# Kernel tuning notes

Measured on AMD Instinct MI355X. Metric: run time of the kernel, lower is better.

## Reference

```python
import math
import jax, jax.numpy as jnp
import numpy as np

B, T, D_MODEL = 4, 2048, 1024
H, HD = 16, 64            # head_dim = d_model // n_heads
NF = 128                  # n_features
EPS = 1e-6
INV_SQRT_NF = 1.0 / math.sqrt(NF)


def make_orf(key, head_dim, n_features, dtype=jnp.float32):
    """Orthogonal Random Features: QR-orthogonalized gaussian blocks, scaled by sqrt(d)."""
    n_blocks = math.ceil(n_features / head_dim)
    keys = jax.random.split(key, n_blocks)
    blocks = []
    for k in keys:
        g = jax.random.normal(k, (head_dim, head_dim), dtype)
        qm, _ = jnp.linalg.qr(g)
        blocks.append(qm)
    W = jnp.concatenate(blocks, axis=1)[:, :n_features]
    return W * jnp.asarray(math.sqrt(head_dim), dtype)


def setup_inputs() -> dict:
    key = jax.random.key(0)
    k0, k1, k2, k3, k4, k5 = jax.random.split(key, 6)
    s = 1.0 / math.sqrt(D_MODEL)  # torch Linear default init scale
    x = jax.random.normal(k0, (B, T, D_MODEL), jnp.float32)
    Wq = jax.random.uniform(k1, (D_MODEL, H * HD), jnp.float32, -s, s)
    Wk = jax.random.uniform(k2, (D_MODEL, H * HD), jnp.float32, -s, s)
    Wv = jax.random.uniform(k3, (D_MODEL, H * HD), jnp.float32, -s, s)
    Wo = jax.random.uniform(k4, (H * HD, D_MODEL), jnp.float32, -s, s)
    W_feat = make_orf(k5, HD, NF)  # (HD, NF), fresh random buffer (not learned)
    return {"x": x, "Wq": Wq, "Wk": Wk, "Wv": Wv, "Wo": Wo, "W_feat": W_feat}


def _favor_plus(x, W):
    """phi(x) = exp(x.W - ||x||^2/2) / sqrt(NF); x:(B,H,T,HD) -> (B,H,T,NF)."""
    sq = 0.5 * jnp.sum(x * x, axis=-1, keepdims=True)
    return jnp.exp(x @ W - sq) * INV_SQRT_NF


def _causal_linear_attention(qp, kp, v):
    """Causal linear attention scan. qp,kp:(B,H,T,NF), v:(B,H,T,HD) -> (B,H,T,HD)."""
    Bb, Hh = qp.shape[0], qp.shape[1]

    def step(carry, qkv):
        S, z = carry  # S:(B,H,NF,HD), z:(B,H,NF)
        q_t, k_t, v_t = qkv
        S = S + jnp.einsum('bhd,bhe->bhde', k_t, v_t)
        z = z + k_t
        num = jnp.einsum('bhd,bhde->bhe', q_t, S)
        den = jnp.einsum('bhd,bhd->bh', q_t, z) + EPS
        return (S, z), num / den[..., None]

    S0 = jnp.zeros((Bb, Hh, NF, HD), qp.dtype)
    z0 = jnp.zeros((Bb, Hh, NF), qp.dtype)
    xs = (jnp.moveaxis(qp, 2, 0), jnp.moveaxis(kp, 2, 0), jnp.moveaxis(v, 2, 0))
    _, ys = jax.lax.scan(step, (S0, z0), xs)  # ys: (T,B,H,HD)
    return jnp.moveaxis(ys, 0, 2)  # (B,H,T,HD)


def reference(x, Wq, Wk, Wv, Wo, W_feat):
    Bb, Tt, _ = x.shape

    def heads(W):
        return (x @ W).reshape(Bb, Tt, H, HD).transpose(0, 2, 1, 3)  # (B,H,T,HD)

    q, k, v = heads(Wq), heads(Wk), heads(Wv)
    qp = _favor_plus(q, W_feat)
    kp = _favor_plus(k, W_feat)
    y = _causal_linear_attention(qp, kp, v)           # (B,H,T,HD)
    y = y.transpose(0, 2, 1, 3).reshape(Bb, Tt, H * HD)
    return y @ Wo
```

## Files before the change

kernel.cpp:

```cpp
#include <hip/hip_runtime.h>
#include <hip/hip_bf16.h>

typedef unsigned int u32;
typedef unsigned short u16;
typedef __bf16 bf16x8 __attribute__((ext_vector_type(8)));
typedef float f32x4 __attribute__((ext_vector_type(4)));

__device__ __forceinline__ float b2f(u16 s){ union{u32 x; float f;} c; c.x = ((u32)s) << 16; return c.f; }
__device__ __forceinline__ float b2f_lo(u32 u){ union{u32 x; float f;} c; c.x = u << 16; return c.f; }
__device__ __forceinline__ float b2f_hi(u32 u){ union{u32 x; float f;} c; c.x = u & 0xFFFF0000u; return c.f; }
__device__ __forceinline__ u16 f2b(float f){
    union{float f; u32 u;} c; c.f = f;
    u32 r = c.u + 0x7FFFu + ((c.u >> 16) & 1u);
    return (u16)(r >> 16);
}
__device__ __forceinline__ u32 pk(float lo, float hi){
    return (u32)f2b(lo) | ((u32)f2b(hi) << 16);
}
__device__ __forceinline__ void gl_lds16(const u16* g, u16* l){
    __builtin_amdgcn_global_load_lds(
        (const __attribute__((address_space(1))) void*)g,
        (__attribute__((address_space(3))) void*)l, 16, 0, 0);
}
#define BARRIER() do { __builtin_amdgcn_s_barrier(); asm volatile("" ::: "memory"); } while(0)
#define SCB __builtin_amdgcn_sched_barrier(0)
#define LD8(p) (*reinterpret_cast<const bf16x8*>(p))
#define SWZP(r) ((((r) ^ ((r) >> 3)) & 7) << 3)


__global__ __launch_bounds__(256) void tobf16(const float* __restrict__ in, u16* __restrict__ out)
{
    size_t i = ((size_t)blockIdx.x * 256 + threadIdx.x) * 8;
    float4 a = *reinterpret_cast<const float4*>(in + i);
    float4 b = *reinterpret_cast<const float4*>(in + i + 4);
    uint4 v; v.x = pk(a.x, a.y); v.y = pk(a.z, a.w); v.z = pk(b.x, b.y); v.w = pk(b.z, b.w);
    *reinterpret_cast<uint4*>(out + i) = v;
}

__global__ __launch_bounds__(256) void transpose_all(const float* __restrict__ Wq, const float* __restrict__ Wk,
                                                     const float* __restrict__ Wv, const float* __restrict__ Wo,
                                                     u16* __restrict__ WTqkv, u16* __restrict__ WTo)
{
    const float* in; u16* out;
    switch (blockIdx.z){
        case 0:  in = Wq; out = WTqkv;           break;
        case 1:  in = Wk; out = WTqkv + 1048576; break;
        case 2:  in = Wv; out = WTqkv + 2097152; break;
        default: in = Wo; out = WTo;             break;
    }
    __shared__ u16 tile[64][72];
    int kb = blockIdx.x * 64, nb = blockIdx.y * 64, tid = threadIdx.x;
#pragma unroll
    for (int i = 0; i < 2; i++){
        int idx = tid + 256*i; int r = idx >> 3; int c8 = (idx & 7) * 8;
        const float* p = &in[(size_t)(kb + r)*1024 + nb + c8];
        float4 lo = *reinterpret_cast<const float4*>(p);
        float4 hi = *reinterpret_cast<const float4*>(p + 4);
        uint4 v;
        v.x = pk(lo.x, lo.y); v.y = pk(lo.z, lo.w);
        v.z = pk(hi.x, hi.y); v.w = pk(hi.z, hi.w);
        *reinterpret_cast<uint4*>(&tile[r][c8]) = v;
    }
    __syncthreads();
#pragma unroll
    for (int i = 0; i < 2; i++){
        int idx = tid + 256*i; int c = idx >> 3; int r8 = (idx & 7) * 8;
        u32 w[4];
#pragma unroll
        for (int j = 0; j < 4; j++)
            w[j] = (u32)tile[r8 + 2*j][c] | ((u32)tile[r8 + 2*j + 1][c] << 16);
        uint4 v; v.x = w[0]; v.y = w[1]; v.z = w[2]; v.w = w[3];
        *reinterpret_cast<uint4*>(&out[(size_t)(nb + c)*1024 + kb + r8]) = v;
    }
}

template<int MODE>
__global__ __launch_bounds__(512, 2) void gemm_1b(const u16* __restrict__ A, const u16* __restrict__ BT,
                                                  float* __restrict__ outf, u16* __restrict__ outh)
{
    __shared__ u16 lds[2][24576];
    const int tid = threadIdx.x;
    const int l = tid & 63, w = tid >> 6;
    const int wr = w >> 2, wc = w & 3;
    const int fr = l & 15, q = l >> 4;
    const int m0 = blockIdx.x * 128, n0 = blockIdx.y * 256;

    const int srow = tid >> 3;
    const int scol = ((tid & 7) ^ (srow & 7)) << 3;
    const u16* Ag = A  + (size_t)(m0 + srow) * 1024 + scol;
    const u16* Bg = BT + (size_t)(n0 + srow) * 1024 + scol;
    const int sd = tid * 8;

    const int colk0 = (q*8)      ^ ((fr & 7) << 3);
    const int colk1 = (32 + q*8) ^ ((fr & 7) << 3);
    const int aoff = (wr*64 + fr) * 64;
    const int boff = 8192 + (wc*64 + fr) * 64;

    f32x4 acc[4][4] = {};

    auto stgA = [&](int buf, int kt){
#pragma unroll
        for (int i = 0; i < 2; ++i)
            gl_lds16(Ag + (size_t)(i*64)*1024 + kt*64, &lds[buf][i*4096 + sd]);
    };
    auto stgB = [&](int buf, int kt){
#pragma unroll
        for (int j = 0; j < 4; ++j)
            gl_lds16(Bg + (size_t)(j*64)*1024 + kt*64, &lds[buf][8192 + j*4096 + sd]);
    };

    stgA(0, 0); stgB(0, 0); stgA(1, 1);
    asm volatile("s_waitcnt vmcnt(2)" ::: "memory");
    SCB;
    BARRIER();

#pragma unroll 1
    for (int uu = 0; uu < 8; ++uu){
#pragma unroll
        for (int par = 0; par < 2; ++par){
            const int u = 2*uu + par;
            u16* Lb = &lds[par][0];
            bf16x8 af[4][2], bf[4][2];

#pragma unroll
            for (int mt = 0; mt < 4; ++mt){
                af[mt][0] = LD8(Lb + aoff + mt*1024 + colk0);
                af[mt][1] = LD8(Lb + aoff + mt*1024 + colk1);
            }
#pragma unroll
            for (int nt = 0; nt < 4; ++nt){
                bf[nt][0] = LD8(Lb + boff + nt*1024 + colk0);
                bf[nt][1] = LD8(Lb + boff + nt*1024 + colk1);
            }
            if (u < 15) stgB(par ^ 1, u + 1);
            if (u < 14) stgA(par, u + 2);

            __builtin_amdgcn_s_setprio(1);
#pragma unroll
            for (int mt = 0; mt < 4; ++mt)
#pragma unroll
                for (int nt = 0; nt < 4; ++nt){
                    acc[mt][nt] = __builtin_amdgcn_mfma_f32_16x16x32_bf16(af[mt][0], bf[nt][0], acc[mt][nt], 0, 0, 0);
                    acc[mt][nt] = __builtin_amdgcn_mfma_f32_16x16x32_bf16(af[mt][1], bf[nt][1], acc[mt][nt], 0, 0, 0);
                }
            __builtin_amdgcn_s_setprio(0);
            SCB;
            if (u < 14){
                asm volatile("s_waitcnt vmcnt(2)" ::: "memory");
                SCB;
                BARRIER();
            } else if (u == 14){
                asm volatile("s_waitcnt vmcnt(0)" ::: "memory");
                SCB;
                BARRIER();
            }
        }
    }

#pragma unroll
    for (int mt = 0; mt < 4; ++mt){
        int row0 = m0 + wr*64 + mt*16 + q*4;
#pragma unroll
        for (int nt = 0; nt < 4; ++nt){
            int col = n0 + wc*64 + nt*16 + fr;
#pragma unroll
            for (int r = 0; r < 4; ++r){
                float val = acc[mt][nt][r];
                int row = row0 + r;
                if (MODE == 2){
                    outf[(size_t)row*1024 + col] = val;
                } else {
                    int which = col >> 10, colw = col & 1023;
                    int h = colw >> 6, d = colw & 63;
                    int bb = row >> 11, tt = row & 2047;
                    outh[(size_t)which*8388608 + (((size_t)(bb*16 + h))*2048 + tt)*64 + d] = f2b(val);
                }
            }
        }
    }
}

__global__ __launch_bounds__(256) void featmap_mfma(const u16* __restrict__ xh, const float* __restrict__ Wf,
                                                    u16* __restrict__ xp)
{
    __shared__ u16 Xl[128][72];
    __shared__ u16 Wft[128][72];
    __shared__ float sqp[128][8];
    __shared__ float sql[128];
    int tid = threadIdx.x;
    int lane = tid & 63, w = tid >> 6;
    int m = lane & 15, q = lane >> 4;
    const u16* xb = xh + (size_t)blockIdx.x * 128 * 64;
#pragma unroll
    for (int it = 0; it < 4; it++){
        int idx = tid + 256*it;
        int row = idx >> 3, c8 = (idx & 7) * 8;
        uint4 v = *reinterpret_cast<const uint4*>(xb + (size_t)row*64 + c8);
        *reinterpret_cast<uint4*>(&Xl[row][c8]) = v;
        u32 ww[4] = {v.x, v.y, v.z, v.w};
        float s = 0.f;
#pragma unroll
        for (int j = 0; j < 4; j++){
            float a = b2f_lo(ww[j]), bb = b2f_hi(ww[j]);
            s += a*a + bb*bb;
        }
        sqp[row][idx & 7] = s;
    }
#pragma unroll
    for (int it = 0; it < 8; it++){
        int idx = tid + 256*it;
        int d = idx >> 5, f4 = (idx & 31) * 4;
        float4 v = *reinterpret_cast<const float4*>(Wf + d*128 + f4);
        Wft[f4+0][d] = f2b(v.x); Wft[f4+1][d] = f2b(v.y);
        Wft[f4+2][d] = f2b(v.z); Wft[f4+3][d] = f2b(v.w);
    }
    __syncthreads();
    if (tid < 128){
        float s = 0.f;
#pragma unroll
        for (int j = 0; j < 8; j++) s += sqp[tid][j];
        sql[tid] = s;
    }
    f32x4 acc[2][8] = {};
#pragma unroll
    for (int ks = 0; ks < 2; ks++){
        bf16x8 af[2], bf[8];
#pragma unroll
        for (int mt = 0; mt < 2; mt++)
            af[mt] = *reinterpret_cast<const bf16x8*>(&Xl[32*w + mt*16 + m][ks*32 + q*8]);
#pragma unroll
        for (int nt = 0; nt < 8; nt++)
            bf[nt] = *reinterpret_cast<const bf16x8*>(&Wft[nt*16 + m][ks*32 + q*8]);
#pragma unroll
        for (int mt = 0; mt < 2; mt++)
#pragma unroll
            for (int nt = 0; nt < 8; nt++)
                acc[mt][nt] = __builtin_amdgcn_mfma_f32_16x16x32_bf16(af[mt], bf[nt], acc[mt][nt], 0, 0, 0);
    }
    __syncthreads();
    const float c = 0.08838834764831845f;
    u16* xpb = xp + (size_t)blockIdx.x * 128 * 128;
#pragma unroll
    for (int mt = 0; mt < 2; mt++){
#pragma unroll
        for (int r = 0; r < 4; r++){
            int t = 32*w + mt*16 + q*4 + r;
            float hs = 0.5f * sql[t];
#pragma unroll
            for (int nt = 0; nt < 8; nt++){
                int f = nt*16 + m;
                xpb[(size_t)t*128 + f] = f2b(__expf(fminf(acc[mt][nt][r] - hs, 60.f)) * c);
            }
        }
    }
}

struct FM1 { u16 Xl[128][72]; u16 Wft[128][72]; };
union  FMU { FM1 p1; u16 Kpt[128][136]; };
__global__ __launch_bounds__(256) void featmap_sum(const u16* __restrict__ kh, const float* __restrict__ Wf,
                                                   const u16* __restrict__ vh, u16* __restrict__ kp,
                                                   u16* __restrict__ Sa, float* __restrict__ zs)
{
    __shared__ FMU sm;
    __shared__ u16 Vt[64][136];
    __shared__ float sqp[128][8];
    __shared__ float sql[128];
    int blk = blockIdx.x, tid = threadIdx.x;
    int lane = tid & 63, w = tid >> 6;
    int m = lane & 15, q = lane >> 4;
    const u16* xb = kh + (size_t)blk * 128 * 64;
    const u16* vb = vh + (size_t)blk * 128 * 64;
#pragma unroll
    for (int it = 0; it < 4; it++){
        int idx = tid + 256*it;
        int row = idx >> 3, c8 = (idx & 7) * 8;
        uint4 v = *reinterpret_cast<const uint4*>(xb + (size_t)row*64 + c8);
        *reinterpret_cast<uint4*>(&sm.p1.Xl[row][c8]) = v;
        u32 ww[4] = {v.x, v.y, v.z, v.w};
        float s = 0.f;
#pragma unroll
        for (int j = 0; j < 4; j++){
            float a = b2f_lo(ww[j]), bb = b2f_hi(ww[j]);
            s += a*a + bb*bb;
        }
        sqp[row][idx & 7] = s;
    }
#pragma unroll
    for (int it = 0; it < 8; it++){
        int idx = tid + 256*it;
        int d = idx >> 5, f4 = (idx & 31) * 4;
        float4 v = *reinterpret_cast<const float4*>(Wf + d*128 + f4);
        sm.p1.Wft[f4+0][d] = f2b(v.x); sm.p1.Wft[f4+1][d] = f2b(v.y);
        sm.p1.Wft[f4+2][d] = f2b(v.z); sm.p1.Wft[f4+3][d] = f2b(v.w);
    }
#pragma unroll
    for (int it = 0; it < 4; it++){
        int idx = tid + 256*it;
        int t = idx >> 3, d8 = (idx & 7)*8;
        uint4 v = *reinterpret_cast<const uint4*>(vb + (size_t)t*64 + d8);
        u32 ww[4] = {v.x, v.y, v.z, v.w};
#pragma unroll
        for (int j = 0; j < 4; j++){
            Vt[d8 + 2*j][t]     = (u16)(ww[j] & 0xFFFFu);
            Vt[d8 + 2*j + 1][t] = (u16)(ww[j] >> 16);
        }
    }
    __syncthreads();
    if (tid < 128){
        float s = 0.f;
#pragma unroll
        for (int j = 0; j < 8; j++) s += sqp[tid][j];
        sql[tid] = s;
    }
    f32x4 acc[2][8] = {};
#pragma unroll
    for (int ks = 0; ks < 2; ks++){
        bf16x8 af[2], bf[8];
#pragma unroll
        for (int mt = 0; mt < 2; mt++)
            af[mt] = *reinterpret_cast<const bf16x8*>(&sm.p1.Xl[32*w + mt*16 + m][ks*32 + q*8]);
#pragma unroll
        for (int nt = 0; nt < 8; nt++)
            bf[nt] = *reinterpret_cast<const bf16x8*>(&sm.p1.Wft[nt*16 + m][ks*32 + q*8]);
#pragma unroll
        for (int mt = 0; mt < 2; mt++)
#pragma unroll
            for (int nt = 0; nt < 8; nt++)
                acc[mt][nt] = __builtin_amdgcn_mfma_f32_16x16x32_bf16(af[mt], bf[nt], acc[mt][nt], 0, 0, 0);
    }
    __syncthreads();
    const float c = 0.08838834764831845f;
    u16* xpb = kp + (size_t)blk * 128 * 128;
#pragma unroll
    for (int mt = 0; mt < 2; mt++){
#pragma unroll
        for (int r = 0; r < 4; r++){
            int t = 32*w + mt*16 + q*4 + r;
            float hs = 0.5f * sql[t];
#pragma unroll
            for (int nt = 0; nt < 8; nt++){
                int f = nt*16 + m;
                u16 pv = f2b(__expf(fminf(acc[mt][nt][r] - hs, 60.f)) * c);
                xpb[(size_t)t*128 + f] = pv;
                sm.Kpt[f][t] = pv;
            }
        }
    }
    __syncthreads();
    f32x4 acc2[8] = {};
#pragma unroll
    for (int ks = 0; ks < 4; ks++){
        bf16x8 af = *reinterpret_cast<const bf16x8*>(&Vt[16*w + m][ks*32 + q*8]);
        bf16x8 bf[8];
#pragma unroll
        for (int nt = 0; nt < 8; nt++)
            bf[nt] = *reinterpret_cast<const bf16x8*>(&sm.Kpt[nt*16 + m][ks*32 + q*8]);
#pragma unroll
        for (int nt = 0; nt < 8; nt++)
            acc2[nt] = __builtin_amdgcn_mfma_f32_16x16x32_bf16(af, bf[nt], acc2[nt], 0, 0, 0);
    }
    u16* Sb = Sa + (size_t)blk*8192;
#pragma unroll
    for (int nt = 0; nt < 8; nt++){
#pragma unroll
        for (int r = 0; r < 4; r++){
            int d = 16*w + q*4 + r;
            int f = nt*16 + m;
            Sb[(size_t)d*128 + f] = f2b(acc2[nt][r]);
        }
    }
    if (tid < 128){
        float z = 0.f;
#pragma unroll
        for (int t = 0; t < 128; t++) z += b2f(sm.Kpt[tid][t]);
        zs[(size_t)blk*128 + tid] = z;
    }
}

__global__ __launch_bounds__(256) void prefix_chunks(const u16* __restrict__ Sa, u16* __restrict__ Sb,
                                                     float* __restrict__ zs)
{
    int bh = blockIdx.x, seg = blockIdx.y, tid = threadIdx.x;
    const u16* src = Sa + (size_t)bh*16*8192;
    u16*       dst = Sb + (size_t)bh*16*8192;
#pragma unroll
    for (int it = 0; it < 4; it++){
        int e = seg*1024 + it*256 + tid;
        float run = 0.f;
#pragma unroll
        for (int c = 0; c < 16; c++){
            float v = b2f(src[(size_t)c*8192 + e]);
            dst[(size_t)c*8192 + e] = f2b(run);
            run += v;
        }
    }
    if (seg == 0 && tid < 128){
        float run = 0.f; float* zp = zs + (size_t)bh*16*128 + tid;
#pragma unroll
        for (int c = 0; c < 16; c++){ float v = zp[c*128]; zp[c*128] = run; run += v; }
    }
}

__global__ __launch_bounds__(512, 4) void chunk_out(const u16* __restrict__ qp, const u16* __restrict__ kp,
                                                    const u16* __restrict__ vh, const u16* __restrict__ St,
                                                    const float* __restrict__ zs, u16* __restrict__ y2d)
{
    __shared__ u16 P[128][128];
    __shared__ u16 Vt[64][128];
    int blk = blockIdx.x, tid = threadIdx.x;
    int lane = tid & 63, w = tid >> 6;
    int m = lane & 15, q = lane >> 4;
    int bh = blk >> 4, c = blk & 15;
    int b = bh >> 4, h = bh & 15, t0 = c*128;
    const u16*  qpb = qp + ((size_t)bh*2048 + t0)*128;
    const u16*  kpb = kp + ((size_t)bh*2048 + t0)*128;
    const u16*  vb  = vh + ((size_t)bh*2048 + t0)*64;
    const u16*  Stb = St + (size_t)blk*8192;
    const float* zsb = zs + (size_t)blk*128;

#pragma unroll
    for (int it = 0; it < 2; it++){
        int idx = tid + 512*it;
        int t = idx >> 3, d8 = (idx & 7)*8;
        uint4 v = *reinterpret_cast<const uint4*>(&vb[(size_t)t*64 + d8]);
        u32 ww[4] = {v.x, v.y, v.z, v.w};
#pragma unroll
        for (int j = 0; j < 4; j++){
            int d0 = d8 + 2*j, d1 = d0 + 1;
            Vt[d0][t ^ SWZP(d0)] = (u16)(ww[j] & 0xFFFFu);
            Vt[d1][t ^ SWZP(d1)] = (u16)(ww[j] >> 16);
        }
    }
    {
        int row = tid >> 2, c4 = tid & 3;
        int i = row >> 4, xr = SWZP(row);
        for (int s2 = 16*(i + 1) + c4*2; s2 < 128; s2 += 8)
            *reinterpret_cast<u32*>(&P[row][s2 ^ xr]) = 0;
    }

    f32x4 acc4[4] = {};
    f32x4 accd = {};
#pragma unroll
    for (int ks = 0; ks < 4; ks++){
        bf16x8 af = LD8(qpb + (size_t)(16*w + m)*128 + ks*32 + q*8);
        float4 z0 = *reinterpret_cast<const float4*>(zsb + ks*32 + q*8);
        float4 z1 = *reinterpret_cast<const float4*>(zsb + ks*32 + q*8 + 4);
        union { u32 u[4]; bf16x8 v; } zc;
        zc.u[0] = pk(z0.x, z0.y); zc.u[1] = pk(z0.z, z0.w);
        zc.u[2] = pk(z1.x, z1.y); zc.u[3] = pk(z1.z, z1.w);
        bf16x8 bf4[4];
#pragma unroll
        for (int nt = 0; nt < 4; nt++)
            bf4[nt] = LD8(Stb + (size_t)(nt*16 + m)*128 + ks*32 + q*8);
#pragma unroll
        for (int nt = 0; nt < 4; nt++)
            acc4[nt] = __builtin_amdgcn_mfma_f32_16x16x32_bf16(af, bf4[nt], acc4[nt], 0, 0, 0);
        accd = __builtin_amdgcn_mfma_f32_16x16x32_bf16(af, zc.v, accd, 0, 0, 0);
    }

    {
        static const unsigned char TIa[36] = {0,1,1,2,2,2,3,3,3,3,4,4,4,4,4,
                                              5,5,5,5,5,5,6,6,6,6,6,6,6,7,7,7,7,7,7,7,7};
        static const unsigned char TJa[36] = {0,0,1,0,1,2,0,1,2,3,0,1,2,3,4,
                                              0,1,2,3,4,5,0,1,2,3,4,5,6,0,1,2,3,4,5,6,7};
        bf16x8 fa[2][4], fb[2][4];
        auto ldtile = [&](int idx, bf16x8* A8, bf16x8* B8){
            int i = TIa[idx], j = TJa[idx];
            const u16* ar = qpb + (size_t)(i*16 + m)*128 + q*8;
            const u16* br = kpb + (size_t)(j*16 + m)*128 + q*8;
#pragma unroll
            for (int ks = 0; ks < 4; ks++){ A8[ks] = LD8(ar + ks*32); B8[ks] = LD8(br + ks*32); }
        };
        auto cptile = [&](int idx, bf16x8* A8, bf16x8* B8){
            f32x4 a = {};
#pragma unroll
            for (int ks = 0; ks < 4; ks++)
                a = __builtin_amdgcn_mfma_f32_16x16x32_bf16(A8[ks], B8[ks], a, 0, 0, 0);
            int i = TIa[idx], j = TJa[idx];
            int scol = j*16 + m;
#pragma unroll
            for (int r = 0; r < 4; r++){
                int trow = i*16 + q*4 + r;
                P[trow][scol ^ SWZP(trow)] = (scol <= trow) ? f2b(a[r]) : (u16)0;
            }
        };
        ldtile(w, fa[0], fb[0]);
#pragma unroll
        for (int itn = 0; itn < 4; ++itn){
            if (itn < 3)      ldtile(w + (itn+1)*8, fa[(itn+1)&1], fb[(itn+1)&1]);
            else if (w < 4)   ldtile(w + 32,        fa[(itn+1)&1], fb[(itn+1)&1]);
            cptile(w + itn*8, fa[itn&1], fb[itn&1]);
        }
        if (w < 4) cptile(w + 32, fa[0], fb[0]);
    }
    __syncthreads();

    bf16x8 ones;
#pragma unroll
    for (int i = 0; i < 8; i++) ones[i] = (__bf16)1.0f;
    {
        int prow = 16*w + m, xp = SWZP(prow);
        int xv[4];
#pragma unroll
        for (int nt = 0; nt < 4; nt++) xv[nt] = SWZP(nt*16 + m);
        for (int ks = 0; ks <= (w >> 1); ks++){
            bf16x8 af = LD8(&P[prow][(ks*32 + q*8) ^ xp]);
            bf16x8 bf4[4];
#pragma unroll
            for (int nt = 0; nt < 4; nt++)
                bf4[nt] = LD8(&Vt[nt*16 + m][(ks*32 + q*8) ^ xv[nt]]);
#pragma unroll
            for (int nt = 0; nt < 4; nt++)
                acc4[nt] = __builtin_amdgcn_mfma_f32_16x16x32_bf16(af, bf4[nt], acc4[nt], 0, 0, 0);
            accd = __builtin_amdgcn_mfma_f32_16x16x32_bf16(af, ones, accd, 0, 0, 0);
        }
    }
#pragma unroll
    for (int nt = 0; nt < 4; nt++){
#pragma unroll
        for (int r = 0; r < 4; r++){
            int t = 16*w + q*4 + r;
            int d = nt*16 + m;
            float den = accd[r] + 1e-6f;
            y2d[((size_t)b*2048 + t0 + t)*1024 + h*64 + d] = f2b(acc4[nt][r] / den);
        }
    }
}

extern "C" void kernel_launch(void* const* d_in, const int* in_sizes, int n_in,
                              void* d_out, int out_size, void* d_ws, size_t ws_size,
                              hipStream_t stream)
{
    (void)in_sizes; (void)n_in; (void)out_size; (void)ws_size;
    const float* x  = (const float*)d_in[0];
    const float* Wq = (const float*)d_in[1];
    const float* Wk = (const float*)d_in[2];
    const float* Wv = (const float*)d_in[3];
    const float* Wo = (const float*)d_in[4];
    const float* Wf = (const float*)d_in[5];
    float* out = (float*)d_out;
    char* ws = (char*)d_ws;

    u16*   xh    = (u16*)  (ws + 0);
    u16*   Sa    = (u16*)  (ws + 0);
    u16*   qh    = (u16*)  (ws + 16777216);
    u16*   Sbp   = (u16*)  (ws + 16777216);
    u16*   kh    = (u16*)  (ws + 33554432);
    u16*   y2d   = (u16*)  (ws + 33554432);
    u16*   vh    = (u16*)  (ws + 50331648);
    u16*   qp    = (u16*)  (ws + 67108864);
    u16*   kp    = (u16*)  (ws + 100663296);
    u16*   WTqkv = (u16*)  (ws + 134217728);
    u16*   WTo   = (u16*)  (ws + 140509184);
    float* zs    = (float*)(ws + 142606336);

    tobf16<<<4096, 256, 0, stream>>>(x, xh);
    transpose_all<<<dim3(16, 16, 4), 256, 0, stream>>>(Wq, Wk, Wv, Wo, WTqkv, WTo);

    gemm_1b<3><<<dim3(64, 12), 512, 0, stream>>>(xh, WTqkv, nullptr, qh);

    featmap_mfma<<<1024, 256, 0, stream>>>(qh, Wf, qp);
    featmap_sum<<<1024, 256, 0, stream>>>(kh, Wf, vh, kp, Sa, zs);

    prefix_chunks<<<dim3(64, 8), 256, 0, stream>>>(Sa, Sbp, zs);
    chunk_out<<<1024, 512, 0, stream>>>(qp, kp, vh, Sbp, zs, y2d);

    gemm_1b<2><<<dim3(64, 4), 512, 0, stream>>>(y2d, WTo, out, nullptr);
}
```

Measured before the change: 283.8 us.

## Stage qp, kp and S chunks in LDS via direct global-to-LDS loads with XOR swizzle

Producer kernels now write qp, kp and the chunk state S with an XOR column swizzle keyed on row. chunk_out bulk-copies its Qp, Kp and St tiles into shared memory using async global_load_lds, then reads MFMA fragments from LDS instead of re-reading global memory for each tile. The goal is to cut redundant global loads, since qp/kp rows were fetched repeatedly across the 36 triangular tiles, and to avoid LDS bank conflicts. The cost is much more LDS per block (about 113KB), and the occupancy hint of 4 is dropped, which reduces concurrent blocks per CU.

```diff
diff --git a/kernel.cpp b/kernel.cpp
--- a/kernel.cpp
+++ b/kernel.cpp
@@ -25,6 +25,7 @@
 #define BARRIER() do { __builtin_amdgcn_s_barrier(); asm volatile("" ::: "memory"); } while(0)
 #define SCB __builtin_amdgcn_sched_barrier(0)
 #define LD8(p) (*reinterpret_cast<const bf16x8*>(p))
+#define SWZR(r) (((r) & 7) << 3)
 #define SWZP(r) ((((r) ^ ((r) >> 3)) & 7) << 3)
 
 
@@ -249,7 +250,7 @@
 #pragma unroll
             for (int nt = 0; nt < 8; nt++){
                 int f = nt*16 + m;
-                xpb[(size_t)t*128 + f] = f2b(__expf(fminf(acc[mt][nt][r] - hs, 60.f)) * c);
+                xpb[(size_t)t*128 + (f ^ SWZR(t))] = f2b(__expf(fminf(acc[mt][nt][r] - hs, 60.f)) * c);
             }
         }
     }
@@ -341,7 +342,7 @@
             for (int nt = 0; nt < 8; nt++){
                 int f = nt*16 + m;
                 u16 pv = f2b(__expf(fminf(acc[mt][nt][r] - hs, 60.f)) * c);
-                xpb[(size_t)t*128 + f] = pv;
+                xpb[(size_t)t*128 + (f ^ SWZR(t))] = pv;
                 sm.Kpt[f][t] = pv;
             }
         }
@@ -366,7 +367,7 @@
         for (int r = 0; r < 4; r++){
             int d = 16*w + q*4 + r;
             int f = nt*16 + m;
-            Sb[(size_t)d*128 + f] = f2b(acc2[nt][r]);
+            Sb[(size_t)d*128 + (f ^ SWZR(d))] = f2b(acc2[nt][r]);
         }
     }
     if (tid < 128){
@@ -401,12 +402,15 @@
     }
 }
 
-__global__ __launch_bounds__(512, 4) void chunk_out(const u16* __restrict__ qp, const u16* __restrict__ kp,
-                                                    const u16* __restrict__ vh, const u16* __restrict__ St,
-                                                    const float* __restrict__ zs, u16* __restrict__ y2d)
-{
+__global__ __launch_bounds__(512) void chunk_out(const u16* __restrict__ qp, const u16* __restrict__ kp,
+                                                 const u16* __restrict__ vh, const u16* __restrict__ St,
+                                                 const float* __restrict__ zs, u16* __restrict__ y2d)
+{
+    __shared__ u16 QpL[16384];
+    __shared__ u16 KpL[16384];
+    __shared__ u16 StL[8192];
+    __shared__ u16 Vt[64][128];
     __shared__ u16 P[128][128];
-    __shared__ u16 Vt[64][128];
     int blk = blockIdx.x, tid = threadIdx.x;
     int lane = tid & 63, w = tid >> 6;
     int m = lane & 15, q = lane >> 4;
@@ -417,32 +421,48 @@
     const u16*  vb  = vh + ((size_t)bh*2048 + t0)*64;
     const u16*  Stb = St + (size_t)blk*8192;
     const float* zsb = zs + (size_t)blk*128;
-
-#pragma unroll
-    for (int it = 0; it < 2; it++){
-        int idx = tid + 512*it;
-        int t = idx >> 3, d8 = (idx & 7)*8;
-        uint4 v = *reinterpret_cast<const uint4*>(&vb[(size_t)t*64 + d8]);
-        u32 ww[4] = {v.x, v.y, v.z, v.w};
-#pragma unroll
-        for (int j = 0; j < 4; j++){
-            int d0 = d8 + 2*j, d1 = d0 + 1;
-            Vt[d0][t ^ SWZP(d0)] = (u16)(ww[j] & 0xFFFFu);
-            Vt[d1][t ^ SWZP(d1)] = (u16)(ww[j] >> 16);
-        }
-    }
+    const int xm8 = SWZR(m);
+    const int sd = tid * 8;
+
+#pragma unroll
+    for (int i = 0; i < 2; ++i) gl_lds16(Stb + i*4096 + sd, StL + i*4096 + sd);
+#pragma unroll
+    for (int i = 0; i < 4; ++i) gl_lds16(qpb + i*4096 + sd, QpL + i*4096 + sd);
+#pragma unroll
+    for (int i = 0; i < 4; ++i) gl_lds16(kpb + i*4096 + sd, KpL + i*4096 + sd);
+    uint4 v0 = *reinterpret_cast<const uint4*>(vb + (size_t)(tid >> 3)*64 + (tid & 7)*8);
+    uint4 v1 = *reinterpret_cast<const uint4*>(vb + (size_t)((tid + 512) >> 3)*64 + (tid & 7)*8);
+
     {
         int row = tid >> 2, c4 = tid & 3;
         int i = row >> 4, xr = SWZP(row);
         for (int s2 = 16*(i + 1) + c4*2; s2 < 128; s2 += 8)
             *reinterpret_cast<u32*>(&P[row][s2 ^ xr]) = 0;
     }
+    SCB;
+    asm volatile("s_waitcnt vmcnt(0)" ::: "memory");
+    SCB;
+    BARRIER();
+
+    {
+        int t = tid >> 3, d8 = (tid & 7)*8;
+        u32 ww0[4] = {v0.x, v0.y, v0.z, v0.w};
+        u32 ww1[4] = {v1.x, v1.y, v1.z, v1.w};
+#pragma unroll
+        for (int j = 0; j < 4; j++){
+            int d0 = d8 + 2*j, d1 = d0 + 1;
+            Vt[d0][t ^ SWZP(d0)]        = (u16)(ww0[j] & 0xFFFFu);
+            Vt[d1][t ^ SWZP(d1)]        = (u16)(ww0[j] >> 16);
+            Vt[d0][(t + 64) ^ SWZP(d0)] = (u16)(ww1[j] & 0xFFFFu);
+            Vt[d1][(t + 64) ^ SWZP(d1)] = (u16)(ww1[j] >> 16);
+        }
+    }
 
     f32x4 acc4[4] = {};
     f32x4 accd = {};
 #pragma unroll
     for (int ks = 0; ks < 4; ks++){
-        bf16x8 af = LD8(qpb + (size_t)(16*w + m)*128 + ks*32 + q*8);
+        bf16x8 af = LD8(QpL + (size_t)(16*w + m)*128 + ((ks*32 + q*8) ^ xm8));
         float4 z0 = *reinterpret_cast<const float4*>(zsb + ks*32 + q*8);
         float4 z1 = *reinterpret_cast<const float4*>(zsb + ks*32 + q*8 + 4);
         union { u32 u[4]; bf16x8 v; } zc;
@@ -451,7 +471,7 @@
         bf16x8 bf4[4];
 #pragma unroll
         for (int nt = 0; nt < 4; nt++)
-            bf4[nt] = LD8(Stb + (size_t)(nt*16 + m)*128 + ks*32 + q*8);
+            bf4[nt] = LD8(StL + (size_t)(nt*16 + m)*128 + ((ks*32 + q*8) ^ xm8));
 #pragma unroll
         for (int nt = 0; nt < 4; nt++)
             acc4[nt] = __builtin_amdgcn_mfma_f32_16x16x32_bf16(af, bf4[nt], acc4[nt], 0, 0, 0);
@@ -463,20 +483,17 @@
                                               5,5,5,5,5,5,6,6,6,6,6,6,6,7,7,7,7,7,7,7,7};
         static const unsigned char TJa[36] = {0,0,1,0,1,2,0,1,2,3,0,1,2,3,4,
                                               0,1,2,3,4,5,0,1,2,3,4,5,6,0,1,2,3,4,5,6,7};
-        bf16x8 fa[2][4], fb[2][4];
-        auto ldtile = [&](int idx, bf16x8* A8, bf16x8* B8){
+        auto dotile = [&](int idx){
             int i = TIa[idx], j = TJa[idx];
-            const u16* ar = qpb + (size_t)(i*16 + m)*128 + q*8;
-            const u16* br = kpb + (size_t)(j*16 + m)*128 + q*8;
-#pragma unroll
-            for (int ks = 0; ks < 4; ks++){ A8[ks] = LD8(ar + ks*32); B8[ks] = LD8(br + ks*32); }
-        };
-        auto cptile = [&](int idx, bf16x8* A8, bf16x8* B8){
+            const u16* ar = QpL + (size_t)(i*16 + m)*128;
+            const u16* br = KpL + (size_t)(j*16 + m)*128;
             f32x4 a = {};
 #pragma unroll
-            for (int ks = 0; ks < 4; ks++)
-                a = __builtin_amdgcn_mfma_f32_16x16x32_bf16(A8[ks], B8[ks], a, 0, 0, 0);
-            int i = TIa[idx], j = TJa[idx];
+            for (int ks = 0; ks < 4; ks++){
+                bf16x8 af = LD8(ar + ((ks*32 + q*8) ^ xm8));
+                bf16x8 bf = LD8(br + ((ks*32 + q*8) ^ xm8));
+                a = __builtin_amdgcn_mfma_f32_16x16x32_bf16(af, bf, a, 0, 0, 0);
+            }
             int scol = j*16 + m;
 #pragma unroll
             for (int r = 0; r < 4; r++){
@@ -484,14 +501,9 @@
                 P[trow][scol ^ SWZP(trow)] = (scol <= trow) ? f2b(a[r]) : (u16)0;
             }
         };
-        ldtile(w, fa[0], fb[0]);
-#pragma unroll
-        for (int itn = 0; itn < 4; ++itn){
-            if (itn < 3)      ldtile(w + (itn+1)*8, fa[(itn+1)&1], fb[(itn+1)&1]);
-            else if (w < 4)   ldtile(w + 32,        fa[(itn+1)&1], fb[(itn+1)&1]);
-            cptile(w + itn*8, fa[itn&1], fb[itn&1]);
-        }
-        if (w < 4) cptile(w + 32, fa[0], fb[0]);
+#pragma unroll
+        for (int itn = 0; itn < 4; ++itn) dotile(w + itn*8);
+        if (w < 4) dotile(w + 32);
     }
     __syncthreads();
 
```

Result: faster. 256.5 us (-9.6%).
